# Kernel tuning notes

Hardware: AMD Instinct MI355X
Metric: run time of the kernel (lower is better)

## Reference

```python
import jax, jax.numpy as jnp
import numpy as np

N_NODES = 100000
DEG = 32
T_CH = 16
N_LAYERS = 2


def setup_inputs() -> dict:
    key = jax.random.key(0)
    k0, k1, k2, k3, k4 = jax.random.split(key, 5)
    # every node has exactly DEG outgoing edges -> degrees all = DEG (log finite)
    src = jnp.repeat(jnp.arange(N_NODES, dtype=jnp.int32), DEG)
    dst = jax.random.randint(k0, (N_NODES * DEG,), 0, N_NODES, dtype=jnp.int32)
    edge_index = jnp.stack([src, dst])  # [2, E]
    x = jax.random.normal(k1, (T_CH, N_NODES), dtype=jnp.float32)
    # per-layer scalar params (shared='all' => shape [1,1] each), stacked over layers
    alpha1 = 2.0 * jax.random.uniform(k2, (N_LAYERS, 1, 1), dtype=jnp.float32) - 1.0
    gamma = 2.0 * jax.random.uniform(k3, (N_LAYERS, 1, 1), dtype=jnp.float32) - 1.0
    bias = 2.0 * jax.random.uniform(k4, (N_LAYERS, 1, 1), dtype=jnp.float32) - 1.0
    return {"x": x, "edge_index": edge_index, "alpha1": alpha1, "gamma": gamma, "bias": bias}


def reference(x, edge_index, alpha1, gamma, bias):
    # x: [T, N]; edge_index: [2, E]; params: [L, 1, 1]
    num_nodes = x.shape[-1]
    src, dst = edge_index[0], edge_index[1]
    deg = jnp.zeros((num_nodes,), x.dtype).at[src].add(jnp.ones((), x.dtype))
    log_deg = jnp.log(deg)[None, :]  # [1, N]
    n_layers = alpha1.shape[0]
    for l in range(n_layers):
        a1, g, b = alpha1[l], gamma[l], bias[l]  # each [1, 1]
        degree_power = jax.nn.sigmoid(g)          # fix_gamma=False
        self_w = jnp.exp(a1)
        # NOTE: source's alpha2 property returns alpha1_param for shared='all' (bug kept)
        neigh_w = self_w * jnp.tanh(a1)
        weighted_repr = x * jnp.exp(degree_power * log_deg)  # [T, N]
        # message: x_j (gathered at src) * exp((gp-1)*log_deg[dst]) * edge_weight(=1)
        edge_w = jnp.exp((degree_power - 1.0) * log_deg[:, dst])  # [1, E]
        msgs = x[:, src] * edge_w                                  # [T, E]
        aggr = jnp.zeros_like(x).at[:, dst].add(msgs)              # scatter-add
        x = self_w * weighted_repr + neigh_w * aggr + b            # with_bias=True
    return x
```

## Files before the change

kernel.cpp:

```cpp
#include <hip/hip_runtime.h>
#include <math.h>

#define N_NODES 100000
#define DEG_E   32
#define T_CH    16
#define E_EDGES (N_NODES * DEG_E)

#define BKT_BITS 8
#define NODES_PER_BKT 256
#define NB 391
#define CAP 9216
#define E_TILE 8192
#define NPART ((E_EDGES + E_TILE - 1) / E_TILE)
#define LOG_DEG 3.4657359027997265f

typedef unsigned int uint;
typedef unsigned short ushort;

static __device__ __forceinline__ uint f2bf(float f) {
    uint u = __float_as_uint(f);
    return (u + 0x7fffu + ((u >> 16) & 1u)) >> 16;
}

static __device__ __forceinline__ void addbf(float* a, uint4 w) {
    a[0] += __uint_as_float(w.x << 16);
    a[1] += __uint_as_float(w.x & 0xffff0000u);
    a[2] += __uint_as_float(w.y << 16);
    a[3] += __uint_as_float(w.y & 0xffff0000u);
    a[4] += __uint_as_float(w.z << 16);
    a[5] += __uint_as_float(w.z & 0xffff0000u);
    a[6] += __uint_as_float(w.w << 16);
    a[7] += __uint_as_float(w.w & 0xffff0000u);
}

__global__ void k_transpose(const float* __restrict__ x, ushort* __restrict__ xt,
                            int* __restrict__ g_cnt) {
    __shared__ float s[64 * 17];
    int tid = threadIdx.x;
    if (blockIdx.x == 0)
        for (int i = tid; i < NB; i += 256) g_cnt[i] = 0;
    int n0 = blockIdx.x * 64;
    int ni = tid & 63, tq = tid >> 6;
    #pragma unroll
    for (int j = 0; j < 4; ++j) {
        int t = tq * 4 + j;
        int n = n0 + ni;
        if (n < N_NODES) s[ni * 17 + t] = x[t * N_NODES + n];
    }
    __syncthreads();
    uint* xw = (uint*)xt;
    for (int j = tid; j < 512; j += 256) {
        int nl = j >> 3, tp = j & 7;
        int n = n0 + nl;
        if (n < N_NODES) {
            uint lo = f2bf(s[nl * 17 + tp * 2]);
            uint hi = f2bf(s[nl * 17 + tp * 2 + 1]);
            xw[n * 8 + tp] = lo | (hi << 16);
        }
    }
}

__global__ void k_partition(const int* __restrict__ dst,
                            int* __restrict__ g_cnt, int* __restrict__ ebuf) {
    __shared__ int s_cnt[NB];
    __shared__ int s_off[NB];
    __shared__ int s_base[NB];
    __shared__ int s_cur[NB];
    __shared__ int s_tile[E_TILE];
    __shared__ int l_cursor;
    int tid = threadIdx.x;
    for (int i = tid; i < NB; i += 256) s_cnt[i] = 0;
    if (tid == 0) l_cursor = 0;
    __syncthreads();

    int e0 = blockIdx.x * E_TILE;
    int n = min(E_TILE, E_EDGES - e0);
    int n4 = n >> 2;
    const int4* d4 = (const int4*)(dst + e0);
    for (int j = tid; j < n4; j += 256) {
        int4 v = d4[j];
        atomicAdd(&s_cnt[v.x >> BKT_BITS], 1);
        atomicAdd(&s_cnt[v.y >> BKT_BITS], 1);
        atomicAdd(&s_cnt[v.z >> BKT_BITS], 1);
        atomicAdd(&s_cnt[v.w >> BKT_BITS], 1);
    }
    __syncthreads();
    for (int i = tid; i < NB; i += 256) {
        int c = s_cnt[i];
        if (c) {
            s_off[i]  = atomicAdd(&l_cursor, c);
            s_base[i] = CAP * i + atomicAdd(&g_cnt[i], c);
        }
        s_cur[i] = 0;
    }
    __syncthreads();
    for (int j = tid; j < n4; j += 256) {
        int4 v = d4[j];
        int de = 4 * j;
        int dd, bkt, p;
        dd = v.x; bkt = dd >> BKT_BITS;
        p = s_off[bkt] + atomicAdd(&s_cur[bkt], 1);
        s_tile[p] = ((de + 0) << 17) | dd;
        dd = v.y; bkt = dd >> BKT_BITS;
        p = s_off[bkt] + atomicAdd(&s_cur[bkt], 1);
        s_tile[p] = ((de + 1) << 17) | dd;
        dd = v.z; bkt = dd >> BKT_BITS;
        p = s_off[bkt] + atomicAdd(&s_cur[bkt], 1);
        s_tile[p] = ((de + 2) << 17) | dd;
        dd = v.w; bkt = dd >> BKT_BITS;
        p = s_off[bkt] + atomicAdd(&s_cur[bkt], 1);
        s_tile[p] = ((de + 3) << 17) | dd;
    }
    __syncthreads();
    for (int j = tid; j < n; j += 256) {
        int v  = s_tile[j];
        int de = v >> 17;
        int dd = v & 0x1FFFF;
        int bkt = dd >> BKT_BITS;
        int srcn = (e0 + de) >> 5;
        ebuf[s_base[bkt] + (j - s_off[bkt])] =
            (srcn << BKT_BITS) | (dd & (NODES_PER_BKT - 1));
    }
}

__global__ void k_sort(const int* __restrict__ g_cnt, int* __restrict__ ebuf,
                       int* __restrict__ node_info) {
    __shared__ int s_pk[CAP];
    __shared__ int s_out[CAP];
    __shared__ int s_cnt[NODES_PER_BKT];
    __shared__ int s_scan[NODES_PER_BKT];
    __shared__ int s_cur[NODES_PER_BKT];
    int b = blockIdx.x;
    int tid = threadIdx.x;
    int base = b * CAP;
    int c = g_cnt[b];

    const int4* v4 = (const int4*)(ebuf + base);
    int c4 = (c + 3) >> 2;
    for (int j = tid; j < c4; j += 256)
        ((int4*)s_pk)[j] = v4[j];
    s_cnt[tid] = 0;
    __syncthreads();
    for (int j = tid; j < c; j += 256)
        atomicAdd(&s_cnt[s_pk[j] & (NODES_PER_BKT - 1)], 1);
    __syncthreads();

    s_scan[tid] = s_cnt[tid];
    __syncthreads();
    for (int off = 1; off < NODES_PER_BKT; off <<= 1) {
        int add = (tid >= off) ? s_scan[tid - off] : 0;
        __syncthreads();
        s_scan[tid] += add;
        __syncthreads();
    }
    int excl = s_scan[tid] - s_cnt[tid];
    s_cur[tid] = excl;

    int nn = (b << BKT_BITS) + tid;
    if (nn < N_NODES) node_info[nn] = excl | (s_cnt[tid] << 16);
    __syncthreads();

    for (int j = tid; j < c; j += 256) {
        int pk = s_pk[j];
        int pos = atomicAdd(&s_cur[pk & (NODES_PER_BKT - 1)], 1);
        s_out[pos] = pk >> BKT_BITS;
    }
    __syncthreads();
    for (int j = tid; j < c; j += 256)
        ebuf[base + j] = s_out[j];
}

template <bool FINAL>
__global__ void k_gather(const ushort* __restrict__ xt,
                         const int* __restrict__ node_info,
                         const int* __restrict__ csr,
                         const float* __restrict__ alpha1,
                         const float* __restrict__ gamma,
                         const float* __restrict__ bias, int layer,
                         void* __restrict__ outp) {
    int tid = blockIdx.x * blockDim.x + threadIdx.x;
    int n = tid >> 3;
    int sub = tid & 7;
    int h = sub & 1;
    int ep = sub >> 1;
    if (n >= N_NODES) return;

    int info = node_info[n];
    int st = (n >> BKT_BITS) * CAP + (info & 0xffff);
    int c  = info >> 16;
    int i0 = (c * ep) >> 2;
    int i1 = (c * (ep + 1)) >> 2;

    const uint4* xv = (const uint4*)xt;
    float acc[8] = {0.f, 0.f, 0.f, 0.f, 0.f, 0.f, 0.f, 0.f};
    int i = i0;
    for (; i + 4 <= i1; i += 4) {
        int s0 = csr[st + i],     s1 = csr[st + i + 1];
        int s2 = csr[st + i + 2], s3 = csr[st + i + 3];
        uint4 w0 = xv[s0 * 2 + h];
        uint4 w1 = xv[s1 * 2 + h];
        uint4 w2 = xv[s2 * 2 + h];
        uint4 w3 = xv[s3 * 2 + h];
        addbf(acc, w0); addbf(acc, w1); addbf(acc, w2); addbf(acc, w3);
    }
    for (; i < i1; ++i) {
        uint4 w = xv[csr[st + i] * 2 + h];
        addbf(acc, w);
    }

    #pragma unroll
    for (int k = 0; k < 8; ++k) {
        acc[k] += __shfl_xor(acc[k], 2, 64);
        acc[k] += __shfl_xor(acc[k], 4, 64);
    }

    float a1 = alpha1[layer];
    float gm = gamma[layer];
    float bb = bias[layer];
    float dp = 1.0f / (1.0f + __expf(-gm));
    float sw = __expf(a1);
    float nw = sw * tanhf(a1);
    float c_self = sw * __expf(dp * LOG_DEG);
    float c_nei  = nw * __expf((dp - 1.0f) * LOG_DEG);

    if (ep == 0) {
        float self[8] = {0.f, 0.f, 0.f, 0.f, 0.f, 0.f, 0.f, 0.f};
        uint4 swd = xv[n * 2 + h];
        addbf(self, swd);

        float o[8];
        #pragma unroll
        for (int k = 0; k < 8; ++k)
            o[k] = c_self * self[k] + c_nei * acc[k] + bb;

        if (FINAL) {
            float* out = (float*)outp;
            int ch0 = h * 8;
            #pragma unroll
            for (int k = 0; k < 8; ++k)
                out[(ch0 + k) * N_NODES + n] = o[k];
        } else {
            uint4 w;
            w.x = f2bf(o[0]) | (f2bf(o[1]) << 16);
            w.y = f2bf(o[2]) | (f2bf(o[3]) << 16);
            w.z = f2bf(o[4]) | (f2bf(o[5]) << 16);
            w.w = f2bf(o[6]) | (f2bf(o[7]) << 16);
            ((uint4*)outp)[n * 2 + h] = w;
        }
    }
}

extern "C" void kernel_launch(void* const* d_in, const int* in_sizes, int n_in,
                              void* d_out, int out_size, void* d_ws, size_t ws_size,
                              hipStream_t stream) {
    const float* x      = (const float*)d_in[0];
    const int*   ei     = (const int*)d_in[1];
    const float* alpha1 = (const float*)d_in[2];
    const float* gamma  = (const float*)d_in[3];
    const float* bias   = (const float*)d_in[4];
    float* out = (float*)d_out;
    const int* dst = ei + E_EDGES;

    const int NT = N_NODES * T_CH;
    ushort* xtA      = (ushort*)d_ws;
    ushort* xtB      = xtA + NT;
    int*   ebuf      = (int*)(xtB + NT);
    int*   node_info = ebuf + NB * CAP;
    int*   g_cnt     = node_info + N_NODES;

    const int B = 256;
    k_transpose<<<(N_NODES + 63) / 64, B, 0, stream>>>(x, xtA, g_cnt);
    k_partition<<<NPART, B, 0, stream>>>(dst, g_cnt, ebuf);
    k_sort<<<NB, B, 0, stream>>>(g_cnt, ebuf, node_info);

    const int grid_g = (N_NODES * 8 + B - 1) / B;
    k_gather<false><<<grid_g, B, 0, stream>>>(
        xtA, node_info, ebuf, alpha1, gamma, bias, 0, (void*)xtB);
    k_gather<true><<<grid_g, B, 0, stream>>>(
        xtB, node_info, ebuf, alpha1, gamma, bias, 1, (void*)out);
}
```

Before: 161.6 us.

## Merge transpose and partition kernels, widen sort blocks, interleave gather edge reads

Fuses the transpose and edge-partition kernels into one launch that picks its role from the block index and shares LDS through a union. The g_cnt zeroing moves to hipMemsetAsync. The sort kernel now runs 512 threads per block and writes its output as int4. The gather kernel interleaves edge indices across its four sub-lanes (stride 4) instead of contiguous quarters, and computes the scalar coefficients only in the lanes that use them. The goal is fewer launches, better overlap of the front stages and better coalescing of the CSR reads. The risks are the extra memset launch and higher LDS use per block in the fused kernel, which can lower occupancy for the transpose blocks.

```diff
diff --git a/kernel.cpp b/kernel.cpp
--- a/kernel.cpp
+++ b/kernel.cpp
@@ -12,6 +12,7 @@
 #define CAP 9216
 #define E_TILE 8192
 #define NPART ((E_EDGES + E_TILE - 1) / E_TILE)
+#define TRANS_BLKS ((N_NODES + 63) / 64)
 #define LOG_DEG 3.4657359027997265f
 
 typedef unsigned int uint;
@@ -33,65 +34,66 @@
     a[7] += __uint_as_float(w.w & 0xffff0000u);
 }
 
-__global__ void k_transpose(const float* __restrict__ x, ushort* __restrict__ xt,
-                            int* __restrict__ g_cnt) {
-    __shared__ float s[64 * 17];
+__global__ void k_front(const float* __restrict__ x, ushort* __restrict__ xt,
+                        const int* __restrict__ dst,
+                        int* __restrict__ g_cnt, int* __restrict__ ebuf) {
+    __shared__ union U {
+        float trans[64 * 17];
+        struct {
+            int cnt[NB]; int off[NB]; int base[NB]; int cur[NB];
+            int tile[E_TILE]; int cursor;
+        } part;
+        __device__ U() {}
+    } u;
     int tid = threadIdx.x;
-    if (blockIdx.x == 0)
-        for (int i = tid; i < NB; i += 256) g_cnt[i] = 0;
-    int n0 = blockIdx.x * 64;
-    int ni = tid & 63, tq = tid >> 6;
-    #pragma unroll
-    for (int j = 0; j < 4; ++j) {
-        int t = tq * 4 + j;
-        int n = n0 + ni;
-        if (n < N_NODES) s[ni * 17 + t] = x[t * N_NODES + n];
-    }
-    __syncthreads();
-    uint* xw = (uint*)xt;
-    for (int j = tid; j < 512; j += 256) {
-        int nl = j >> 3, tp = j & 7;
-        int n = n0 + nl;
-        if (n < N_NODES) {
-            uint lo = f2bf(s[nl * 17 + tp * 2]);
-            uint hi = f2bf(s[nl * 17 + tp * 2 + 1]);
-            xw[n * 8 + tp] = lo | (hi << 16);
-        }
-    }
-}
-
-__global__ void k_partition(const int* __restrict__ dst,
-                            int* __restrict__ g_cnt, int* __restrict__ ebuf) {
-    __shared__ int s_cnt[NB];
-    __shared__ int s_off[NB];
-    __shared__ int s_base[NB];
-    __shared__ int s_cur[NB];
-    __shared__ int s_tile[E_TILE];
-    __shared__ int l_cursor;
-    int tid = threadIdx.x;
-    for (int i = tid; i < NB; i += 256) s_cnt[i] = 0;
-    if (tid == 0) l_cursor = 0;
-    __syncthreads();
-
-    int e0 = blockIdx.x * E_TILE;
+
+    if (blockIdx.x < TRANS_BLKS) {
+        int n0 = blockIdx.x * 64;
+        int ni = tid & 63, tq = tid >> 6;
+        #pragma unroll
+        for (int j = 0; j < 4; ++j) {
+            int t = tq * 4 + j;
+            int n = n0 + ni;
+            if (n < N_NODES) u.trans[ni * 17 + t] = x[t * N_NODES + n];
+        }
+        __syncthreads();
+        uint* xw = (uint*)xt;
+        for (int j = tid; j < 512; j += 256) {
+            int nl = j >> 3, tp = j & 7;
+            int n = n0 + nl;
+            if (n < N_NODES) {
+                uint lo = f2bf(u.trans[nl * 17 + tp * 2]);
+                uint hi = f2bf(u.trans[nl * 17 + tp * 2 + 1]);
+                xw[n * 8 + tp] = lo | (hi << 16);
+            }
+        }
+        return;
+    }
+
+    int pb = blockIdx.x - TRANS_BLKS;
+    for (int i = tid; i < NB; i += 256) u.part.cnt[i] = 0;
+    if (tid == 0) u.part.cursor = 0;
+    __syncthreads();
+
+    int e0 = pb * E_TILE;
     int n = min(E_TILE, E_EDGES - e0);
     int n4 = n >> 2;
     const int4* d4 = (const int4*)(dst + e0);
     for (int j = tid; j < n4; j += 256) {
         int4 v = d4[j];
-        atomicAdd(&s_cnt[v.x >> BKT_BITS], 1);
-        atomicAdd(&s_cnt[v.y >> BKT_BITS], 1);
-        atomicAdd(&s_cnt[v.z >> BKT_BITS], 1);
-        atomicAdd(&s_cnt[v.w >> BKT_BITS], 1);
+        atomicAdd(&u.part.cnt[v.x >> BKT_BITS], 1);
+        atomicAdd(&u.part.cnt[v.y >> BKT_BITS], 1);
+        atomicAdd(&u.part.cnt[v.z >> BKT_BITS], 1);
+        atomicAdd(&u.part.cnt[v.w >> BKT_BITS], 1);
     }
     __syncthreads();
     for (int i = tid; i < NB; i += 256) {
-        int c = s_cnt[i];
+        int c = u.part.cnt[i];
         if (c) {
-            s_off[i]  = atomicAdd(&l_cursor, c);
-            s_base[i] = CAP * i + atomicAdd(&g_cnt[i], c);
-        }
-        s_cur[i] = 0;
+            u.part.off[i]  = atomicAdd(&u.part.cursor, c);
+            u.part.base[i] = CAP * i + atomicAdd(&g_cnt[i], c);
+        }
+        u.part.cur[i] = 0;
     }
     __syncthreads();
     for (int j = tid; j < n4; j += 256) {
@@ -99,26 +101,26 @@
         int de = 4 * j;
         int dd, bkt, p;
         dd = v.x; bkt = dd >> BKT_BITS;
-        p = s_off[bkt] + atomicAdd(&s_cur[bkt], 1);
-        s_tile[p] = ((de + 0) << 17) | dd;
+        p = u.part.off[bkt] + atomicAdd(&u.part.cur[bkt], 1);
+        u.part.tile[p] = ((de + 0) << 17) | dd;
         dd = v.y; bkt = dd >> BKT_BITS;
-        p = s_off[bkt] + atomicAdd(&s_cur[bkt], 1);
-        s_tile[p] = ((de + 1) << 17) | dd;
+        p = u.part.off[bkt] + atomicAdd(&u.part.cur[bkt], 1);
+        u.part.tile[p] = ((de + 1) << 17) | dd;
         dd = v.z; bkt = dd >> BKT_BITS;
-        p = s_off[bkt] + atomicAdd(&s_cur[bkt], 1);
-        s_tile[p] = ((de + 2) << 17) | dd;
+        p = u.part.off[bkt] + atomicAdd(&u.part.cur[bkt], 1);
+        u.part.tile[p] = ((de + 2) << 17) | dd;
         dd = v.w; bkt = dd >> BKT_BITS;
-        p = s_off[bkt] + atomicAdd(&s_cur[bkt], 1);
-        s_tile[p] = ((de + 3) << 17) | dd;
+        p = u.part.off[bkt] + atomicAdd(&u.part.cur[bkt], 1);
+        u.part.tile[p] = ((de + 3) << 17) | dd;
     }
     __syncthreads();
     for (int j = tid; j < n; j += 256) {
-        int v  = s_tile[j];
+        int v  = u.part.tile[j];
         int de = v >> 17;
         int dd = v & 0x1FFFF;
         int bkt = dd >> BKT_BITS;
         int srcn = (e0 + de) >> 5;
-        ebuf[s_base[bkt] + (j - s_off[bkt])] =
+        ebuf[u.part.base[bkt] + (j - u.part.off[bkt])] =
             (srcn << BKT_BITS) | (dd & (NODES_PER_BKT - 1));
     }
 }
@@ -137,37 +139,39 @@
 
     const int4* v4 = (const int4*)(ebuf + base);
     int c4 = (c + 3) >> 2;
-    for (int j = tid; j < c4; j += 256)
+    for (int j = tid; j < c4; j += 512)
         ((int4*)s_pk)[j] = v4[j];
-    s_cnt[tid] = 0;
-    __syncthreads();
-    for (int j = tid; j < c; j += 256)
+    if (tid < NODES_PER_BKT) s_cnt[tid] = 0;
+    __syncthreads();
+    for (int j = tid; j < c; j += 512)
         atomicAdd(&s_cnt[s_pk[j] & (NODES_PER_BKT - 1)], 1);
     __syncthreads();
 
-    s_scan[tid] = s_cnt[tid];
+    if (tid < NODES_PER_BKT) s_scan[tid] = s_cnt[tid];
     __syncthreads();
     for (int off = 1; off < NODES_PER_BKT; off <<= 1) {
-        int add = (tid >= off) ? s_scan[tid - off] : 0;
+        int add = 0;
+        if (tid < NODES_PER_BKT && tid >= off) add = s_scan[tid - off];
         __syncthreads();
-        s_scan[tid] += add;
+        if (tid < NODES_PER_BKT) s_scan[tid] += add;
         __syncthreads();
     }
-    int excl = s_scan[tid] - s_cnt[tid];
-    s_cur[tid] = excl;
-
-    int nn = (b << BKT_BITS) + tid;
-    if (nn < N_NODES) node_info[nn] = excl | (s_cnt[tid] << 16);
-    __syncthreads();
-
-    for (int j = tid; j < c; j += 256) {
+    if (tid < NODES_PER_BKT) {
+        int excl = s_scan[tid] - s_cnt[tid];
+        s_cur[tid] = excl;
+        int nn = (b << BKT_BITS) + tid;
+        if (nn < N_NODES) node_info[nn] = excl | (s_cnt[tid] << 16);
+    }
+    __syncthreads();
+
+    for (int j = tid; j < c; j += 512) {
         int pk = s_pk[j];
         int pos = atomicAdd(&s_cur[pk & (NODES_PER_BKT - 1)], 1);
         s_out[pos] = pk >> BKT_BITS;
     }
     __syncthreads();
-    for (int j = tid; j < c; j += 256)
-        ebuf[base + j] = s_out[j];
+    for (int j = tid; j < c4; j += 512)
+        ((int4*)(ebuf + base))[j] = ((const int4*)s_out)[j];
 }
 
 template <bool FINAL>
@@ -188,22 +192,20 @@
     int info = node_info[n];
     int st = (n >> BKT_BITS) * CAP + (info & 0xffff);
     int c  = info >> 16;
-    int i0 = (c * ep) >> 2;
-    int i1 = (c * (ep + 1)) >> 2;
 
     const uint4* xv = (const uint4*)xt;
     float acc[8] = {0.f, 0.f, 0.f, 0.f, 0.f, 0.f, 0.f, 0.f};
-    int i = i0;
-    for (; i + 4 <= i1; i += 4) {
-        int s0 = csr[st + i],     s1 = csr[st + i + 1];
-        int s2 = csr[st + i + 2], s3 = csr[st + i + 3];
+    int i = ep;
+    for (; i + 12 < c; i += 16) {
+        int s0 = csr[st + i],     s1 = csr[st + i + 4];
+        int s2 = csr[st + i + 8], s3 = csr[st + i + 12];
         uint4 w0 = xv[s0 * 2 + h];
         uint4 w1 = xv[s1 * 2 + h];
         uint4 w2 = xv[s2 * 2 + h];
         uint4 w3 = xv[s3 * 2 + h];
         addbf(acc, w0); addbf(acc, w1); addbf(acc, w2); addbf(acc, w3);
     }
-    for (; i < i1; ++i) {
+    for (; i < c; i += 4) {
         uint4 w = xv[csr[st + i] * 2 + h];
         addbf(acc, w);
     }
@@ -214,16 +216,16 @@
         acc[k] += __shfl_xor(acc[k], 4, 64);
     }
 
-    float a1 = alpha1[layer];
-    float gm = gamma[layer];
-    float bb = bias[layer];
-    float dp = 1.0f / (1.0f + __expf(-gm));
-    float sw = __expf(a1);
-    float nw = sw * tanhf(a1);
-    float c_self = sw * __expf(dp * LOG_DEG);
-    float c_nei  = nw * __expf((dp - 1.0f) * LOG_DEG);
-
     if (ep == 0) {
+        float a1 = alpha1[layer];
+        float gm = gamma[layer];
+        float bb = bias[layer];
+        float dp = 1.0f / (1.0f + __expf(-gm));
+        float sw = __expf(a1);
+        float nw = sw * tanhf(a1);
+        float c_self = sw * __expf(dp * LOG_DEG);
+        float c_nei  = nw * __expf((dp - 1.0f) * LOG_DEG);
+
         float self[8] = {0.f, 0.f, 0.f, 0.f, 0.f, 0.f, 0.f, 0.f};
         uint4 swd = xv[n * 2 + h];
         addbf(self, swd);
@@ -269,9 +271,9 @@
     int*   g_cnt     = node_info + N_NODES;
 
     const int B = 256;
-    k_transpose<<<(N_NODES + 63) / 64, B, 0, stream>>>(x, xtA, g_cnt);
-    k_partition<<<NPART, B, 0, stream>>>(dst, g_cnt, ebuf);
-    k_sort<<<NB, B, 0, stream>>>(g_cnt, ebuf, node_info);
+    hipMemsetAsync(g_cnt, 0, NB * sizeof(int), stream);
+    k_front<<<TRANS_BLKS + NPART, B, 0, stream>>>(x, xtA, dst, g_cnt, ebuf);
+    k_sort<<<NB, 512, 0, stream>>>(g_cnt, ebuf, node_info);
 
     const int grid_g = (N_NODES * 8 + B - 1) / B;
     k_gather<false><<<grid_g, B, 0, stream>>>(
```

New measurement: 160.9 us. About the same (-0.4%).
